# Kernel tuning notes

Measured on AMD Instinct MI355X. Metric: run time of the kernel, lower is better.

## Reference

```python
import jax, jax.numpy as jnp
import numpy as np

HEADS, HDIM, GROUPS, EPS = 8, 64, 8, 1e-5

def setup_inputs() -> dict:
    key = jax.random.key(0)
    ks = jax.random.split(key, 3)
    c, inner = 256, HEADS * HDIM
    return {
        "x": jax.random.normal(ks[0], (2, c, 16, 16, 16), dtype=jnp.float32),
        "gamma": jnp.ones((c,), jnp.float32),
        "beta": jnp.zeros((c,), jnp.float32),
        "w_qkv": jax.random.normal(ks[1], (3 * inner, c), dtype=jnp.float32) * (c ** -0.5),
        "b_qkv": jnp.zeros((3 * inner,), jnp.float32),
        "w_out": jax.random.normal(ks[2], (c, inner), dtype=jnp.float32) * (inner ** -0.5),
        "b_out": jnp.zeros((c,), jnp.float32),
    }

def reference(x, gamma, beta, w_qkv, b_qkv, w_out, b_out):
    b, c, d, h, w = x.shape
    n = d * h * w
    scale = HDIM ** -0.5
    # GroupNorm(8, c)
    xg = x.reshape(b, GROUPS, c // GROUPS, d, h, w)
    mu = xg.mean(axis=(2, 3, 4, 5), keepdims=True)
    var = xg.var(axis=(2, 3, 4, 5), keepdims=True)
    xn = ((xg - mu) * jax.lax.rsqrt(var + EPS)).reshape(b, c, d, h, w)
    xn = xn * gamma[None, :, None, None, None] + beta[None, :, None, None, None]
    # 1x1x1 conv -> qkv, channel order (three, heads, dim)
    qkv = jnp.einsum('oc,bcdhw->bodhw', w_qkv, xn) + b_qkv[None, :, None, None, None]
    qkv = qkv.reshape(b, 3, HEADS, HDIM, n).transpose(1, 0, 2, 4, 3)  # [3,b,heads,n,dim]
    q, k, v = qkv[0], qkv[1], qkv[2]
    attn = jax.nn.softmax(jnp.einsum('bhnd,bhmd->bhnm', q, k) * scale, axis=-1)
    out = jnp.einsum('bhnm,bhmd->bhnd', attn, v)  # [b,heads,n,dim]
    out = out.transpose(0, 1, 3, 2).reshape(b, HEADS * HDIM, d, h, w)  # (heads dim) channels
    y = jnp.einsum('oc,bcdhw->bodhw', w_out, out) + b_out[None, :, None, None, None]
    # Dropout(0.1) in eval mode = identity
    return y + x
```

## Files before the change

### kernel.cpp

```cpp
#include <hip/hip_runtime.h>
#include <hip/hip_bf16.h>


typedef __attribute__((ext_vector_type(8))) short bf8_t;
typedef __attribute__((ext_vector_type(4))) float f4_t;
typedef __attribute__((ext_vector_type(16))) float f16v;

#define NTOK 4096
#define GRP_ELEMS (32 * 4096)

__device__ __forceinline__ unsigned short f2bf(float f) {
  union { float f; unsigned int i; } v; v.f = f;
  unsigned int r = v.i + 0x7fffu + ((v.i >> 16) & 1u);
  return (unsigned short)(r >> 16);
}

__device__ __forceinline__ unsigned int pkbf(float a, float b) {
  float2 t; t.x = a; t.y = b;
  __hip_bfloat162 h = __float22bfloat162_rn(t);
  union { __hip_bfloat162 h; unsigned int u; } c; c.h = h;
  return c.u;
}

__device__ __forceinline__ void gl_lds16(const unsigned short* g, unsigned short* l) {
  __builtin_amdgcn_global_load_lds((const __attribute__((address_space(1))) void*)g,
                                   (__attribute__((address_space(3))) void*)l, 16, 0, 0);
}

__device__ __forceinline__ bf8_t ldsw128(const unsigned short* base, int row, int du) {
  return *(const bf8_t*)((const char*)base + (((row << 7) + (du << 4)) ^ ((row & 7) << 4)));
}
__device__ __forceinline__ bf8_t ldsw64(const unsigned short* base, int row, int du) {
  return *(const bf8_t*)((const char*)base + (((row << 6) + (du << 4)) ^ (((row >> 1) & 3) << 4)));
}

#if __has_builtin(__builtin_amdgcn_exp2f)
#define EXP2 __builtin_amdgcn_exp2f
#else
#define EXP2 exp2f
#endif

__global__ __launch_bounds__(256) void gn_stats_castw(const float* __restrict__ x, float* __restrict__ stats,
    const float* __restrict__ wqkv, const float* __restrict__ wout,
    unsigned short* __restrict__ wq, unsigned short* __restrict__ wo) {
  int bid = blockIdx.x;
  if (bid >= 256) {
    int i = (bid - 256) * 256 + threadIdx.x;
    const float* src; unsigned short* dst; int off;
    if (i < 98304) { src = wqkv; dst = wq; off = i; }
    else           { src = wout; dst = wo; off = i - 98304; }
    float4 v = ((const float4*)src)[off];
    union { unsigned short s[4]; uint2 u; } o;
    o.s[0] = f2bf(v.x); o.s[1] = f2bf(v.y); o.s[2] = f2bf(v.z); o.s[3] = f2bf(v.w);
    *(uint2*)(dst + (size_t)off * 4) = o.u;
    return;
  }
  int g = bid & 15, sp = bid >> 4;
  const float4* p = (const float4*)(x + (size_t)g * GRP_ELEMS + (size_t)sp * 8192);
  float s = 0.f, s2 = 0.f;
  for (int i = threadIdx.x; i < 2048; i += 256) {
    float4 v = p[i];
    s  += v.x + v.y + v.z + v.w;
    s2 += v.x * v.x + v.y * v.y + v.z * v.z + v.w * v.w;
  }
  for (int m = 32; m; m >>= 1) { s += __shfl_xor(s, m); s2 += __shfl_xor(s2, m); }
  __shared__ float rs[4][2];
  int wv = threadIdx.x >> 6;
  if ((threadIdx.x & 63) == 0) { rs[wv][0] = s; rs[wv][1] = s2; }
  __syncthreads();
  if (threadIdx.x == 0) {
    float ts = rs[0][0] + rs[1][0] + rs[2][0] + rs[3][0];
    float t2 = rs[0][1] + rs[1][1] + rs[2][1] + rs[3][1];
    atomicAdd(&stats[g], ts);
    atomicAdd(&stats[16 + g], t2);
  }
}

__global__ __launch_bounds__(256) void gn_apply(const float* __restrict__ x,
    const float* __restrict__ gamma, const float* __restrict__ beta,
    const float* __restrict__ stats, unsigned short* __restrict__ xnt) {
  __shared__ float t[64][65];
  int b = blockIdx.z, c0 = blockIdx.y * 64, n0 = blockIdx.x * 64;
  int tr = threadIdx.x >> 2;
  int tc = (threadIdx.x & 3) * 16;
  int c = c0 + tr;
  int g = b * 8 + (c >> 5);
  float mu = stats[g] * (1.f / GRP_ELEMS);
  float var = stats[16 + g] * (1.f / GRP_ELEMS) - mu * mu;
  float rstd = rsqrtf(var + 1e-5f);
  float sc = gamma[c] * rstd;
  float sh = beta[c] - mu * sc;
  const float* xp = x + ((size_t)(b * 256 + c)) * NTOK + n0 + tc;
  for (int q = 0; q < 4; ++q) {
    float4 v = *(const float4*)(xp + q * 4);
    t[tr][tc + q * 4 + 0] = v.x * sc + sh;
    t[tr][tc + q * 4 + 1] = v.y * sc + sh;
    t[tr][tc + q * 4 + 2] = v.z * sc + sh;
    t[tr][tc + q * 4 + 3] = v.w * sc + sh;
  }
  __syncthreads();
  int n = n0 + tr;
  union { unsigned short s[16]; uint4 u[2]; } tmp;
  for (int q = 0; q < 16; ++q) tmp.s[q] = f2bf(t[tc + q][tr]);
  uint4* dst = (uint4*)(xnt + ((size_t)b * NTOK + n) * 256 + c0 + tc);
  dst[0] = tmp.u[0];
  dst[1] = tmp.u[1];
}

__global__ __launch_bounds__(256) void qkv_gemm(const unsigned short* __restrict__ wq,
    const unsigned short* __restrict__ xnt, const float* __restrict__ bqkv,
    unsigned short* __restrict__ Qg, unsigned short* __restrict__ Kg, unsigned short* __restrict__ Vt) {
  __shared__ unsigned short Al[2][4096];
  __shared__ unsigned short Bl[2][4096];
  int b = blockIdx.z, m0 = blockIdx.y * 128, n0 = blockIdx.x * 128;
  const unsigned short* Ap = wq + (size_t)m0 * 256;
  const unsigned short* Bp = xnt + ((size_t)b * NTOK + n0) * 256;
  int lane = threadIdx.x & 63, wv = threadIdx.x >> 6;
  int lq = lane & 15, hq = lane >> 4;
  int m_off = (wv >> 1) * 64, n_off = (wv & 1) * 64;
  f4_t acc[4][4] = {};
  {
    for (int is = 0; is < 2; ++is) {
      int ck = wv * 128 + is * 64 + lane;
      int r = ck >> 2, cu = ck & 3;
      int csw = (cu ^ ((r >> 1) & 3)) << 3;
      gl_lds16(Ap + (size_t)r * 256 + csw, &Al[0][(wv * 128 + is * 64) * 8]);
      gl_lds16(Bp + (size_t)r * 256 + csw, &Bl[0][(wv * 128 + is * 64) * 8]);
    }
  }
  __syncthreads();
  for (int kt = 0; kt < 8; ++kt) {
    int cb = kt & 1, nb = cb ^ 1;
    if (kt < 7) {
      int k0 = (kt + 1) * 32;
      for (int is = 0; is < 2; ++is) {
        int ck = wv * 128 + is * 64 + lane;
        int r = ck >> 2, cu = ck & 3;
        int csw = (cu ^ ((r >> 1) & 3)) << 3;
        gl_lds16(Ap + (size_t)r * 256 + k0 + csw, &Al[nb][(wv * 128 + is * 64) * 8]);
        gl_lds16(Bp + (size_t)r * 256 + k0 + csw, &Bl[nb][(wv * 128 + is * 64) * 8]);
      }
    }
    const unsigned short* Ac = Al[cb];
    const unsigned short* Bc = Bl[cb];
    bf8_t af[4], bfr[4];
    for (int i = 0; i < 4; ++i) af[i]  = ldsw64(Ac, m_off + i * 16 + lq, hq);
    for (int j = 0; j < 4; ++j) bfr[j] = ldsw64(Bc, n_off + j * 16 + lq, hq);
    for (int i = 0; i < 4; ++i)
      for (int j = 0; j < 4; ++j)
        acc[i][j] = __builtin_amdgcn_mfma_f32_16x16x32_bf16(af[i], bfr[j], acc[i][j], 0, 0, 0);
    __syncthreads();
  }
  int tq = m0 >> 9;
  if (tq < 2) {
    unsigned short* dst = tq == 0 ? Qg : Kg;
    float sc = tq == 0 ? 0.1803368801111243f : 1.0f;
    for (int i = 0; i < 4; ++i)
      for (int j = 0; j < 4; ++j) {
        int o0 = m0 + m_off + i * 16 + hq * 4;
        int n = n0 + n_off + j * 16 + lq;
        int h = (o0 >> 6) & 7, dd0 = o0 & 63;
        size_t bh = (size_t)b * 8 + h;
        uint2 pk;
        pk.x = pkbf((acc[i][j][0] + bqkv[o0 + 0]) * sc, (acc[i][j][1] + bqkv[o0 + 1]) * sc);
        pk.y = pkbf((acc[i][j][2] + bqkv[o0 + 2]) * sc, (acc[i][j][3] + bqkv[o0 + 3]) * sc);
        *(uint2*)(dst + (bh * NTOK + n) * 64 + dd0) = pk;
      }
  } else {
    for (int i = 0; i < 4; ++i)
      for (int j = 0; j < 4; ++j) {
        int n = n0 + n_off + j * 16 + lq;
        for (int jj = 0; jj < 4; ++jj) {
          int o = m0 + m_off + i * 16 + hq * 4 + jj;
          int h = (o >> 6) & 7, dd = o & 63;
          size_t bh = (size_t)b * 8 + h;
          Vt[(bh * 64 + dd) * NTOK + n] = f2bf(acc[i][j][jj] + bqkv[o]);
        }
      }
  }
}

__global__ __launch_bounds__(256, 4) void attn(const unsigned short* __restrict__ Qg,
    const unsigned short* __restrict__ Kg, const unsigned short* __restrict__ Vt,
    unsigned short* __restrict__ att) {
  __shared__ char smem[32768];
  int bid = blockIdx.x;
  int inner = bid >> 3;
  int bh = (bid & 7) * 2 + (inner & 1);
  int q0 = (inner >> 1) * 64;
  int b = bh >> 3, h = bh & 7;
  const unsigned short* kp = Kg + (size_t)bh * NTOK * 64;
  const unsigned short* vp = Vt + (size_t)bh * 64 * NTOK;
  int tid = threadIdx.x;
  int lane = tid & 63, wv = tid >> 6;
  int l31 = lane & 31, h5 = lane >> 5;
  int strip = wv & 1, half = wv >> 1;
  int kvbase = half * 2048;

  const unsigned short* qp = Qg + ((size_t)bh * NTOK + q0 + strip * 32 + l31) * 64;
  bf8_t aq[4];
  #pragma unroll
  for (int sl = 0; sl < 4; ++sl)
    aq[sl] = *(const bf8_t*)(qp + sl * 16 + h5 * 8);

  unsigned short* Kb0 = (unsigned short*)(smem + half * 8192);
  unsigned short* Vb0 = (unsigned short*)(smem + 16384 + half * 8192);

  int t128 = tid & 127;
  int kr = t128 >> 3, kc = t128 & 7;
  int vr = t128 >> 2, vc = t128 & 3;
  const unsigned short* kSrc = kp + (size_t)(kvbase + kr) * 64 + ((kc ^ (kr & 7)) << 3);
  const unsigned short* vSrc = vp + (size_t)vr * NTOK + kvbase + ((vc ^ ((vr >> 1) & 3)) << 3);
  unsigned short* kDst0 = Kb0 + t128 * 8;
  unsigned short* vDst0 = Vb0 + t128 * 8;

#define STAGE(BUF) do { \
    gl_lds16(kSrc,          kDst0 + (BUF) * 2048); \
    gl_lds16(kSrc + 1024,   kDst0 + (BUF) * 2048 + 1024); \
    gl_lds16(vSrc,          vDst0 + (BUF) * 2048); \
    gl_lds16(vSrc + 131072, vDst0 + (BUF) * 2048 + 1024); \
    kSrc += 2048; vSrc += 32; \
  } while (0)

  f16v accO[2] = {};
  float ls = 0.f;

#define COMPUTE(CB) do { \
    const unsigned short* Kc = Kb0 + (CB) * 2048; \
    const unsigned short* Vc = Vb0 + (CB) * 2048; \
    f16v s = {}; \
    __builtin_amdgcn_s_setprio(1); \
    _Pragma("unroll") \
    for (int sl = 0; sl < 4; ++sl) { \
      bf8_t ak = ldsw128(Kc, l31, sl * 2 + h5); \
      s = __builtin_amdgcn_mfma_f32_32x32x16_bf16(ak, aq[sl], s, 0, 0, 0); \
    } \
    __builtin_amdgcn_s_setprio(0); \
    float rs = 0.f; \
    _Pragma("unroll") \
    for (int r = 0; r < 16; ++r) { float p = EXP2(s[r]); s[r] = p; rs += p; } \
    ls += rs; \
    _Pragma("unroll") \
    for (int tp = 0; tp < 2; ++tp) { \
      unsigned int g0a = pkbf(s[8 * tp + 0], s[8 * tp + 1]); \
      unsigned int g0b = pkbf(s[8 * tp + 2], s[8 * tp + 3]); \
      unsigned int g1a = pkbf(s[8 * tp + 4], s[8 * tp + 5]); \
      unsigned int g1b = pkbf(s[8 * tp + 6], s[8 * tp + 7]); \
      unsigned int ra = __shfl_xor(h5 ? g0a : g1a, 32); \
      unsigned int rb = __shfl_xor(h5 ? g0b : g1b, 32); \
      union { unsigned int u[4]; bf8_t v; } pb; \
      pb.u[0] = h5 ? ra : g0a;  pb.u[1] = h5 ? rb : g0b; \
      pb.u[2] = h5 ? g1a : ra;  pb.u[3] = h5 ? g1b : rb; \
      bf8_t av0 = ldsw64(Vc, l31, tp * 2 + h5); \
      bf8_t av1 = ldsw64(Vc, 32 + l31, tp * 2 + h5); \
      __builtin_amdgcn_s_setprio(1); \
      accO[0] = __builtin_amdgcn_mfma_f32_32x32x16_bf16(av0, pb.v, accO[0], 0, 0, 0); \
      accO[1] = __builtin_amdgcn_mfma_f32_32x32x16_bf16(av1, pb.v, accO[1], 0, 0, 0); \
      __builtin_amdgcn_s_setprio(0); \
    } \
  } while (0)

  STAGE(0);
  __syncthreads();
  for (int tt = 0; tt < 31; ++tt) {
    STAGE(1); COMPUTE(0); __syncthreads();
    STAGE(0); COMPUTE(1); __syncthreads();
  }
  STAGE(1); COMPUTE(0); __syncthreads();
  COMPUTE(1); __syncthreads();

  ls += __shfl_xor(ls, 32);

  float* cbuf = (float*)(smem);
  float* lbuf = (float*)(smem + 18432);
  if (half == 1) {
    float* dst = cbuf + strip * 2304 + lane * 36;
    #pragma unroll
    for (int db = 0; db < 2; ++db)
      #pragma unroll
      for (int g = 0; g < 4; ++g) {
        float4 v; v.x = accO[db][4 * g + 0]; v.y = accO[db][4 * g + 1];
        v.z = accO[db][4 * g + 2]; v.w = accO[db][4 * g + 3];
        *(float4*)(dst + (db * 4 + g) * 4) = v;
      }
    lbuf[strip * 64 + lane] = ls;
  }
  __syncthreads();
  if (half == 0) {
    const float* src = cbuf + strip * 2304 + lane * 36;
    float lt = ls + lbuf[strip * 64 + lane];
    float inv = 1.0f / lt;
    int q = q0 + strip * 32 + l31;
    unsigned short* op = att + ((size_t)b * NTOK + q) * 512 + h * 64;
    #pragma unroll
    for (int db = 0; db < 2; ++db)
      #pragma unroll
      for (int g = 0; g < 4; ++g) {
        float4 v = *(const float4*)(src + (db * 4 + g) * 4);
        uint2 pk;
        pk.x = pkbf((accO[db][4 * g + 0] + v.x) * inv, (accO[db][4 * g + 1] + v.y) * inv);
        pk.y = pkbf((accO[db][4 * g + 2] + v.z) * inv, (accO[db][4 * g + 3] + v.w) * inv);
        *(uint2*)(op + db * 32 + g * 8 + h5 * 4) = pk;
      }
  }
#undef COMPUTE
#undef STAGE
}

__global__ __launch_bounds__(256) void out_proj(const unsigned short* __restrict__ wo,
    const unsigned short* __restrict__ att, const float* __restrict__ bout,
    const float* __restrict__ x, float* __restrict__ y) {
  __shared__ unsigned short Al[2][2048];
  __shared__ unsigned short Bl[2][2048];
  int b = blockIdx.z, m0 = blockIdx.y * 64, n0 = blockIdx.x * 64;
  const unsigned short* Ap = wo + (size_t)m0 * 512;
  const unsigned short* Bp = att + ((size_t)b * NTOK + n0) * 512;
  int lane = threadIdx.x & 63, wv = threadIdx.x >> 6;
  int lq = lane & 15, hq = lane >> 4;
  int m_off = (wv >> 1) * 32, n_off = (wv & 1) * 32;
  int ck = threadIdx.x;
  int rr = ck >> 2, cu = ck & 3;
  int csw = (cu ^ ((rr >> 1) & 3)) << 3;
  f4_t acc[2][2] = {};
  {
    gl_lds16(Ap + (size_t)rr * 512 + csw, &Al[0][ck * 8]);
    gl_lds16(Bp + (size_t)rr * 512 + csw, &Bl[0][ck * 8]);
  }
  __syncthreads();
  for (int kt = 0; kt < 16; ++kt) {
    int cb = kt & 1, nb = cb ^ 1;
    if (kt < 15) {
      int k0 = (kt + 1) * 32;
      gl_lds16(Ap + (size_t)rr * 512 + k0 + csw, &Al[nb][ck * 8]);
      gl_lds16(Bp + (size_t)rr * 512 + k0 + csw, &Bl[nb][ck * 8]);
    }
    const unsigned short* Ac = Al[cb];
    const unsigned short* Bc = Bl[cb];
    bf8_t af[2], bfr[2];
    for (int i = 0; i < 2; ++i) af[i]  = ldsw64(Ac, m_off + i * 16 + lq, hq);
    for (int jj = 0; jj < 2; ++jj) bfr[jj] = ldsw64(Bc, n_off + jj * 16 + lq, hq);
    for (int i = 0; i < 2; ++i)
      for (int jj = 0; jj < 2; ++jj)
        acc[i][jj] = __builtin_amdgcn_mfma_f32_16x16x32_bf16(af[i], bfr[jj], acc[i][jj], 0, 0, 0);
    __syncthreads();
  }
  for (int i = 0; i < 2; ++i)
    for (int jj = 0; jj < 2; ++jj) {
      int n = n0 + n_off + jj * 16 + lq;
      for (int e = 0; e < 4; ++e) {
        int co = m0 + m_off + i * 16 + hq * 4 + e;
        size_t idx = ((size_t)b * 256 + co) * NTOK + n;
        y[idx] = acc[i][jj][e] + bout[co] + x[idx];
      }
    }
}

extern "C" void kernel_launch(void* const* d_in, const int* in_sizes, int n_in,
                              void* d_out, int out_size, void* d_ws, size_t ws_size,
                              hipStream_t stream) {
  const float* x     = (const float*)d_in[0];
  const float* gamma = (const float*)d_in[1];
  const float* beta  = (const float*)d_in[2];
  const float* wqkv  = (const float*)d_in[3];
  const float* bqkv  = (const float*)d_in[4];
  const float* wout  = (const float*)d_in[5];
  const float* bout  = (const float*)d_in[6];
  float* y = (float*)d_out;

  char* ws = (char*)d_ws;
  float*          stats = (float*)ws;
  unsigned short* WQ    = (unsigned short*)(ws + 256);
  unsigned short* WO    = (unsigned short*)(ws + 786688);
  unsigned short* XNT   = (unsigned short*)(ws + 1048832);
  unsigned short* Qg    = (unsigned short*)(ws + 5243136);
  unsigned short* Kg    = (unsigned short*)(ws + 13631744);
  unsigned short* Vt    = (unsigned short*)(ws + 22020352);
  unsigned short* ATT   = (unsigned short*)(ws + 30408960);

  hipMemsetAsync(stats, 0, 128, stream);
  gn_stats_castw<<<768, 256, 0, stream>>>(x, stats, wqkv, wout, WQ, WO);
  gn_apply<<<dim3(64, 4, 2), 256, 0, stream>>>(x, gamma, beta, stats, XNT);
  qkv_gemm<<<dim3(32, 12, 2), 256, 0, stream>>>(WQ, XNT, bqkv, Qg, Kg, Vt);
  attn<<<1024, 256, 0, stream>>>(Qg, Kg, Vt, ATT);
  out_proj<<<dim3(64, 4, 2), 256, 0, stream>>>(WO, ATT, bout, x, y);
}
```

Before: 206.2 us.

## Transpose V in separate kernel, use permlane swap and MFMA row-sum in attention

The QKV GEMM now writes V in the same row-major layout as Q and K, and a new small transpose kernel produces Vt. This replaces the scattered 2-byte stores in the GEMM epilogue. In the attention kernel, the cross-half shuffle is replaced by v_permlane32_swap, and the LDS swizzle offsets are precomputed once. The softmax denominator is now accumulated by an extra MFMA against a ones vector instead of scalar adds. The cost is an extra kernel launch, an extra round trip of V through memory, and one more MFMA per tile.

```diff
diff --git a/kernel.cpp b/kernel.cpp
--- a/kernel.cpp
+++ b/kernel.cpp
@@ -22,14 +22,15 @@
   return c.u;
 }
 
+__device__ __forceinline__ void plswap(unsigned int& a, unsigned int& b) {
+  asm volatile("v_permlane32_swap_b32 %0, %1" : "+v"(a), "+v"(b));
+}
+
 __device__ __forceinline__ void gl_lds16(const unsigned short* g, unsigned short* l) {
   __builtin_amdgcn_global_load_lds((const __attribute__((address_space(1))) void*)g,
                                    (__attribute__((address_space(3))) void*)l, 16, 0, 0);
 }
 
-__device__ __forceinline__ bf8_t ldsw128(const unsigned short* base, int row, int du) {
-  return *(const bf8_t*)((const char*)base + (((row << 7) + (du << 4)) ^ ((row & 7) << 4)));
-}
 __device__ __forceinline__ bf8_t ldsw64(const unsigned short* base, int row, int du) {
   return *(const bf8_t*)((const char*)base + (((row << 6) + (du << 4)) ^ (((row >> 1) & 3) << 4)));
 }
@@ -109,7 +110,7 @@
 
 __global__ __launch_bounds__(256) void qkv_gemm(const unsigned short* __restrict__ wq,
     const unsigned short* __restrict__ xnt, const float* __restrict__ bqkv,
-    unsigned short* __restrict__ Qg, unsigned short* __restrict__ Kg, unsigned short* __restrict__ Vt) {
+    unsigned short* __restrict__ Qg, unsigned short* __restrict__ Kg, unsigned short* __restrict__ Vn) {
   __shared__ unsigned short Al[2][4096];
   __shared__ unsigned short Bl[2][4096];
   int b = blockIdx.z, m0 = blockIdx.y * 128, n0 = blockIdx.x * 128;
@@ -152,38 +153,44 @@
     __syncthreads();
   }
   int tq = m0 >> 9;
-  if (tq < 2) {
-    unsigned short* dst = tq == 0 ? Qg : Kg;
-    float sc = tq == 0 ? 0.1803368801111243f : 1.0f;
-    for (int i = 0; i < 4; ++i)
-      for (int j = 0; j < 4; ++j) {
-        int o0 = m0 + m_off + i * 16 + hq * 4;
-        int n = n0 + n_off + j * 16 + lq;
-        int h = (o0 >> 6) & 7, dd0 = o0 & 63;
-        size_t bh = (size_t)b * 8 + h;
-        uint2 pk;
-        pk.x = pkbf((acc[i][j][0] + bqkv[o0 + 0]) * sc, (acc[i][j][1] + bqkv[o0 + 1]) * sc);
-        pk.y = pkbf((acc[i][j][2] + bqkv[o0 + 2]) * sc, (acc[i][j][3] + bqkv[o0 + 3]) * sc);
-        *(uint2*)(dst + (bh * NTOK + n) * 64 + dd0) = pk;
-      }
-  } else {
-    for (int i = 0; i < 4; ++i)
-      for (int j = 0; j < 4; ++j) {
-        int n = n0 + n_off + j * 16 + lq;
-        for (int jj = 0; jj < 4; ++jj) {
-          int o = m0 + m_off + i * 16 + hq * 4 + jj;
-          int h = (o >> 6) & 7, dd = o & 63;
-          size_t bh = (size_t)b * 8 + h;
-          Vt[(bh * 64 + dd) * NTOK + n] = f2bf(acc[i][j][jj] + bqkv[o]);
-        }
-      }
-  }
+  unsigned short* dst = tq == 0 ? Qg : (tq == 1 ? Kg : Vn);
+  float sc = tq == 0 ? 0.1803368801111243f : 1.0f;
+  for (int i = 0; i < 4; ++i)
+    for (int j = 0; j < 4; ++j) {
+      int o0 = m0 + m_off + i * 16 + hq * 4;
+      int n = n0 + n_off + j * 16 + lq;
+      int h = (o0 >> 6) & 7, dd0 = o0 & 63;
+      size_t bh = (size_t)b * 8 + h;
+      uint2 pk;
+      pk.x = pkbf((acc[i][j][0] + bqkv[o0 + 0]) * sc, (acc[i][j][1] + bqkv[o0 + 1]) * sc);
+      pk.y = pkbf((acc[i][j][2] + bqkv[o0 + 2]) * sc, (acc[i][j][3] + bqkv[o0 + 3]) * sc);
+      *(uint2*)(dst + (bh * NTOK + n) * 64 + dd0) = pk;
+    }
+}
+
+__global__ __launch_bounds__(256) void vt_tr(const unsigned short* __restrict__ Vn,
+                                             unsigned short* __restrict__ Vt) {
+  __shared__ unsigned short t[64][72];
+  int bh = blockIdx.y, n0 = blockIdx.x * 64;
+  int tr = threadIdx.x >> 2, qc = (threadIdx.x & 3) * 16;
+  const unsigned short* src = Vn + ((size_t)bh * NTOK + n0 + tr) * 64 + qc;
+  uint4 v0 = *(const uint4*)src;
+  uint4 v1 = *(const uint4*)(src + 8);
+  *(uint4*)&t[tr][qc] = v0;
+  *(uint4*)&t[tr][qc + 8] = v1;
+  __syncthreads();
+  union { unsigned short s[16]; uint4 u[2]; } o;
+  #pragma unroll
+  for (int j = 0; j < 16; ++j) o.s[j] = t[qc + j][tr];
+  unsigned short* dst = Vt + ((size_t)bh * 64 + tr) * NTOK + n0 + qc;
+  *(uint4*)dst = o.u[0];
+  *(uint4*)(dst + 8) = o.u[1];
 }
 
 __global__ __launch_bounds__(256, 4) void attn(const unsigned short* __restrict__ Qg,
     const unsigned short* __restrict__ Kg, const unsigned short* __restrict__ Vt,
     unsigned short* __restrict__ att) {
-  __shared__ char smem[32768];
+  __shared__ __align__(16) char smem[32768];
   int bid = blockIdx.x;
   int inner = bid >> 3;
   int bh = (bid & 7) * 2 + (inner & 1);
@@ -206,6 +213,25 @@
   unsigned short* Kb0 = (unsigned short*)(smem + half * 8192);
   unsigned short* Vb0 = (unsigned short*)(smem + 16384 + half * 8192);
 
+  int koff[4];
+  #pragma unroll
+  for (int sl = 0; sl < 4; ++sl)
+    koff[sl] = ((l31 << 7) + ((sl * 2 + h5) << 4)) ^ ((l31 & 7) << 4);
+  int voff[2][2];
+  #pragma unroll
+  for (int tp = 0; tp < 2; ++tp)
+    #pragma unroll
+    for (int db = 0; db < 2; ++db) {
+      int row = db * 32 + l31;
+      voff[tp][db] = ((row << 6) + ((tp * 2 + h5) << 4)) ^ (((row >> 1) & 3) << 4);
+    }
+
+  bf8_t ones;
+  { union { unsigned short s[8]; bf8_t v; } o;
+    #pragma unroll
+    for (int j = 0; j < 8; ++j) o.s[j] = 0x3f80;
+    ones = o.v; }
+
   int t128 = tid & 127;
   int kr = t128 >> 3, kc = t128 & 7;
   int vr = t128 >> 2, vc = t128 & 3;
@@ -223,39 +249,37 @@
   } while (0)
 
   f16v accO[2] = {};
-  float ls = 0.f;
+  f16v accDen = {};
 
 #define COMPUTE(CB) do { \
-    const unsigned short* Kc = Kb0 + (CB) * 2048; \
-    const unsigned short* Vc = Vb0 + (CB) * 2048; \
+    const char* Kc = (const char*)Kb0 + (CB) * 4096; \
+    const char* Vc = (const char*)Vb0 + (CB) * 4096; \
     f16v s = {}; \
     __builtin_amdgcn_s_setprio(1); \
     _Pragma("unroll") \
     for (int sl = 0; sl < 4; ++sl) { \
-      bf8_t ak = ldsw128(Kc, l31, sl * 2 + h5); \
+      bf8_t ak = *(const bf8_t*)(Kc + koff[sl]); \
       s = __builtin_amdgcn_mfma_f32_32x32x16_bf16(ak, aq[sl], s, 0, 0, 0); \
     } \
     __builtin_amdgcn_s_setprio(0); \
-    float rs = 0.f; \
     _Pragma("unroll") \
-    for (int r = 0; r < 16; ++r) { float p = EXP2(s[r]); s[r] = p; rs += p; } \
-    ls += rs; \
+    for (int r = 0; r < 16; ++r) s[r] = EXP2(s[r]); \
     _Pragma("unroll") \
     for (int tp = 0; tp < 2; ++tp) { \
-      unsigned int g0a = pkbf(s[8 * tp + 0], s[8 * tp + 1]); \
-      unsigned int g0b = pkbf(s[8 * tp + 2], s[8 * tp + 3]); \
-      unsigned int g1a = pkbf(s[8 * tp + 4], s[8 * tp + 5]); \
-      unsigned int g1b = pkbf(s[8 * tp + 6], s[8 * tp + 7]); \
-      unsigned int ra = __shfl_xor(h5 ? g0a : g1a, 32); \
-      unsigned int rb = __shfl_xor(h5 ? g0b : g1b, 32); \
+      unsigned int a0 = pkbf(s[8 * tp + 0], s[8 * tp + 1]); \
+      unsigned int b0 = pkbf(s[8 * tp + 2], s[8 * tp + 3]); \
+      unsigned int a1 = pkbf(s[8 * tp + 4], s[8 * tp + 5]); \
+      unsigned int b1 = pkbf(s[8 * tp + 6], s[8 * tp + 7]); \
+      plswap(a0, a1); \
+      plswap(b0, b1); \
       union { unsigned int u[4]; bf8_t v; } pb; \
-      pb.u[0] = h5 ? ra : g0a;  pb.u[1] = h5 ? rb : g0b; \
-      pb.u[2] = h5 ? g1a : ra;  pb.u[3] = h5 ? g1b : rb; \
-      bf8_t av0 = ldsw64(Vc, l31, tp * 2 + h5); \
-      bf8_t av1 = ldsw64(Vc, 32 + l31, tp * 2 + h5); \
+      pb.u[0] = a0; pb.u[1] = b0; pb.u[2] = a1; pb.u[3] = b1; \
+      bf8_t av0 = *(const bf8_t*)(Vc + voff[tp][0]); \
+      bf8_t av1 = *(const bf8_t*)(Vc + voff[tp][1]); \
       __builtin_amdgcn_s_setprio(1); \
       accO[0] = __builtin_amdgcn_mfma_f32_32x32x16_bf16(av0, pb.v, accO[0], 0, 0, 0); \
       accO[1] = __builtin_amdgcn_mfma_f32_32x32x16_bf16(av1, pb.v, accO[1], 0, 0, 0); \
+      accDen  = __builtin_amdgcn_mfma_f32_32x32x16_bf16(ones, pb.v, accDen, 0, 0, 0); \
       __builtin_amdgcn_s_setprio(0); \
     } \
   } while (0)
@@ -269,7 +293,7 @@
   STAGE(1); COMPUTE(0); __syncthreads();
   COMPUTE(1); __syncthreads();
 
-  ls += __shfl_xor(ls, 32);
+  float ls = accDen[0];
 
   float* cbuf = (float*)(smem);
   float* lbuf = (float*)(smem + 18432);
@@ -376,11 +400,13 @@
   unsigned short* Kg    = (unsigned short*)(ws + 13631744);
   unsigned short* Vt    = (unsigned short*)(ws + 22020352);
   unsigned short* ATT   = (unsigned short*)(ws + 30408960);
+  unsigned short* Vn    = ATT;
 
   hipMemsetAsync(stats, 0, 128, stream);
   gn_stats_castw<<<768, 256, 0, stream>>>(x, stats, wqkv, wout, WQ, WO);
   gn_apply<<<dim3(64, 4, 2), 256, 0, stream>>>(x, gamma, beta, stats, XNT);
-  qkv_gemm<<<dim3(32, 12, 2), 256, 0, stream>>>(WQ, XNT, bqkv, Qg, Kg, Vt);
+  qkv_gemm<<<dim3(32, 12, 2), 256, 0, stream>>>(WQ, XNT, bqkv, Qg, Kg, Vn);
+  vt_tr<<<dim3(64, 16), 256, 0, stream>>>(Vn, Vt);
   attn<<<1024, 256, 0, stream>>>(Qg, Kg, Vt, ATT);
   out_proj<<<dim3(64, 4, 2), 256, 0, stream>>>(WO, ATT, bout, x, y);
 }
```

Result: no change. 207.9 us (+0.9%).
